# Optimization experiments

Measured on AMD Instinct MI355X. Metric: run time of the kernel, lower is better.

The kernel has to match this reference:

```python
import jax, jax.numpy as jnp
import numpy as np

V, H, L, NH, DH, FF, P, T = 21128, 768, 12, 12, 64, 3072, 512, 9
B, S = 16, 256
EPS = 1e-12

def _ln(x, g, b):
    m = x.mean(-1, keepdims=True)
    v = ((x - m) ** 2).mean(-1, keepdims=True)
    return (x - m) * jax.lax.rsqrt(v + EPS) * g + b

def setup_inputs() -> dict:
    key = jax.random.key(0)
    ks = iter(jax.random.split(key, 64))
    def nrm(shape, s=0.02):
        return (jax.random.normal(next(ks), shape, jnp.float32) * s)
    inp = {
        'input_ids': jax.random.randint(next(ks), (B, 1, S), 0, V, dtype=jnp.int32),
        'token_type_ids': jnp.zeros((B, 1, S), jnp.int32),
        'attention_mask': jnp.ones((B, 1, S), jnp.int32),
        'tags': jax.random.randint(next(ks), (B, S), 0, T, dtype=jnp.int32),
        'word_emb': nrm((V, H)), 'pos_emb': nrm((P, H)), 'type_emb': nrm((2, H)),
        'emb_ln_g': jnp.ones((H,), jnp.float32), 'emb_ln_b': jnp.zeros((H,), jnp.float32),
        'Wq': nrm((L, H, H)), 'bq': jnp.zeros((L, H), jnp.float32),
        'Wk': nrm((L, H, H)), 'bk': jnp.zeros((L, H), jnp.float32),
        'Wv': nrm((L, H, H)), 'bv': jnp.zeros((L, H), jnp.float32),
        'Wo': nrm((L, H, H)), 'bo': jnp.zeros((L, H), jnp.float32),
        'ln1_g': jnp.ones((L, H), jnp.float32), 'ln1_b': jnp.zeros((L, H), jnp.float32),
        'W1': nrm((L, H, FF)), 'b1': jnp.zeros((L, FF), jnp.float32),
        'W2': nrm((L, FF, H)), 'b2': jnp.zeros((L, H), jnp.float32),
        'ln2_g': jnp.ones((L, H), jnp.float32), 'ln2_b': jnp.zeros((L, H), jnp.float32),
        'dense_W': nrm((H, T)), 'dense_b': jnp.zeros((T,), jnp.float32),
        'crf_start': nrm((T,), 0.1), 'crf_end': nrm((T,), 0.1), 'crf_trans': nrm((T, T), 0.1),
    }
    return inp

def _model(input_ids, token_type_ids, attention_mask, tags,
           word_emb, pos_emb, type_emb, emb_ln_g, emb_ln_b,
           Wq, bq, Wk, bk, Wv, bv, Wo, bo, ln1_g, ln1_b,
           W1, b1, W2, b2, ln2_g, ln2_b, dense_W, dense_b,
           crf_start, crf_end, crf_trans):
    ids = input_ids[:, 0, :]            # [B,S]
    tt = token_type_ids[:, 0, :]
    amask = attention_mask[:, 0, :]     # [B,S] int
    Bn, Sn = ids.shape
    # --- BERT embeddings (post-LN BERT-base) ---
    x = word_emb[ids] + pos_emb[:Sn][None, :, :] + type_emb[tt]
    x = _ln(x, emb_ln_g, emb_ln_b)
    bias = jnp.where(amask[:, None, None, :] > 0, 0.0, -1e9).astype(x.dtype)  # [B,1,1,S]
    scale = 1.0 / np.sqrt(DH).astype(np.float32)
    def layer(h, p):
        wq, bq_, wk, bk_, wv, bv_, wo, bo_, g1, c1, w1, d1, w2, d2, g2, c2 = p
        q = (h @ wq + bq_).reshape(Bn, Sn, NH, DH).transpose(0, 2, 1, 3)
        k = (h @ wk + bk_).reshape(Bn, Sn, NH, DH).transpose(0, 2, 1, 3)
        v = (h @ wv + bv_).reshape(Bn, Sn, NH, DH).transpose(0, 2, 1, 3)
        att = jax.nn.softmax(jnp.einsum('bhqd,bhkd->bhqk', q, k) * scale + bias, axis=-1)
        ctx = jnp.einsum('bhqk,bhkd->bhqd', att, v).transpose(0, 2, 1, 3).reshape(Bn, Sn, H)
        h = _ln(h + ctx @ wo + bo_, g1, c1)
        ff = jax.nn.gelu(h @ w1 + d1, approximate=False)
        h = _ln(h + ff @ w2 + d2, g2, c2)
        return h, None
    x, _ = jax.lax.scan(layer, x, (Wq, bq, Wk, bk, Wv, bv, Wo, bo, ln1_g, ln1_b, W1, b1, W2, b2, ln2_g, ln2_b))
    # --- emission head, seq-first like the torch code ---
    emis = (x @ dense_W + dense_b).transpose(1, 0, 2)   # [S,B,T]
    m = (amask.T > 0)                                    # [S,B] bool
    tags_sb = tags.T                                     # [S,B]
    bidx = jnp.arange(Bn)
    # --- CRF numerator (gold path score) ---
    score0 = crf_start[tags_sb[0]] + emis[0, bidx, tags_sb[0]]
    def num_step(sc, inp):
        e, t, tp, mm = inp
        inc = crf_trans[tp, t] + e[bidx, t]
        return sc + jnp.where(mm, inc, 0.0), None
    score, _ = jax.lax.scan(num_step, score0, (emis[1:], tags_sb[1:], tags_sb[:-1], m[1:]))
    lengths = m.astype(jnp.int32).sum(0)                 # [B]
    last_tag = jnp.take_along_axis(tags_sb, (lengths - 1)[None, :], axis=0)[0]
    score = score + crf_end[last_tag]
    # --- CRF partition (forward algorithm) ---
    alpha0 = crf_start[None, :] + emis[0]                # [B,T]
    def fwd_step(a, inp):
        e, mm = inp
        nxt = jax.nn.logsumexp(a[:, :, None] + crf_trans[None, :, :] + e[:, None, :], axis=1)
        return jnp.where(mm[:, None], nxt, a), None
    alpha, _ = jax.lax.scan(fwd_step, alpha0, (emis[1:], m[1:]))
    logZ = jax.nn.logsumexp(alpha + crf_end[None, :], axis=-1)
    loss = -(score - logZ).mean()                        # reduction='mean'
    # --- Viterbi decode ---
    v0 = crf_start[None, :] + emis[0]
    tid = jnp.arange(T)
    def vit_step(vv, inp):
        e, mm = inp
        sc = vv[:, :, None] + crf_trans[None, :, :]       # [B,T,T]
        nv = sc.max(1) + e
        idx = sc.argmax(1).astype(jnp.int32)
        vv2 = jnp.where(mm[:, None], nv, vv)
        idx = jnp.where(mm[:, None], idx, tid[None, :].astype(jnp.int32))
        return vv2, idx
    vfin, hist = jax.lax.scan(vit_step, v0, (emis[1:], m[1:]))  # hist: [S-1,B,T]
    last = jnp.argmax(vfin + crf_end[None, :], axis=-1).astype(jnp.int32)  # [B]
    def back_step(t, h):
        prev = jnp.take_along_axis(h, t[:, None], axis=1)[:, 0]
        return prev, prev
    _, path = jax.lax.scan(back_step, last, hist, reverse=True)  # [S-1,B]
    preds = jnp.concatenate([path, last[None, :]], axis=0).T     # [B,S]
    return loss, preds

def reference(input_ids, token_type_ids, attention_mask, tags,
              word_emb, pos_emb, type_emb, emb_ln_g, emb_ln_b,
              Wq, bq, Wk, bk, Wv, bv, Wo, bo, ln1_g, ln1_b,
              W1, b1, W2, b2, ln2_g, ln2_b, dense_W, dense_b,
              crf_start, crf_end, crf_trans):
    return _model(input_ids, token_type_ids, attention_mask, tags,
                  word_emb, pos_emb, type_emb, emb_ln_g, emb_ln_b,
                  Wq, bq, Wk, bk, Wv, bv, Wo, bo, ln1_g, ln1_b,
                  W1, b1, W2, b2, ln2_g, ln2_b, dense_W, dense_b,
                  crf_start, crf_end, crf_trans)
```

## Files before the change

### kernel.cpp

```cpp
#include <hip/hip_runtime.h>
#include <math.h>

#define B_ 16
#define S_ 256
#define H_ 768
#define L_ 12
#define NH_ 12
#define DH_ 64
#define FF_ 3072
#define T_ 9

typedef unsigned short ushort_t;
typedef __attribute__((ext_vector_type(8))) __bf16 bf16x8;
typedef __attribute__((ext_vector_type(4))) float f32x4;
typedef __attribute__((ext_vector_type(4))) unsigned short us4;
typedef __attribute__((ext_vector_type(8))) unsigned short us8;
typedef __attribute__((ext_vector_type(4))) unsigned int u32x4;

__device__ __forceinline__ ushort_t f2bf(float f) {
  union { float f; unsigned u; } v; v.f = f;
  unsigned r = v.u + 0x7FFFu + ((v.u >> 16) & 1u);
  return (ushort_t)(r >> 16);
}
__device__ __forceinline__ float bf2f(ushort_t h) {
  union { unsigned u; float f; } v; v.u = ((unsigned)h) << 16;
  return v.f;
}
__device__ __forceinline__ float rdlane(float v, int l) {
  union { float f; int i; } u; u.f = v;
  union { int i; float f; } o; o.i = __builtin_amdgcn_readlane(u.i, l);
  return o.f;
}
__device__ __forceinline__ void gload16(const void* g, void* l) {
  __builtin_amdgcn_global_load_lds((const __attribute__((address_space(1))) void*)g,
                                   (__attribute__((address_space(3))) void*)l, 16, 0, 0);
}

__global__ __launch_bounds__(256) void emb_ln_kernel(const int* __restrict__ ids, const int* __restrict__ tt,
                              const float* __restrict__ we, const float* __restrict__ pe,
                              const float* __restrict__ te, const float* __restrict__ g,
                              const float* __restrict__ bb,
                              ushort_t* __restrict__ oh, ushort_t* __restrict__ ol) {
  const int token = blockIdx.x;
  const int tid = threadIdx.x;
  const int s = token & (S_ - 1);
  const int id = ids[token];
  const int t2 = tt[token];
  float x[3];
  float sum = 0.f;
#pragma unroll
  for (int i = 0; i < 3; ++i) {
    int d = tid + i * 256;
    x[i] = we[(size_t)id * H_ + d] + pe[(size_t)s * H_ + d] + te[(size_t)t2 * H_ + d];
    sum += x[i];
  }
  __shared__ float red[4];
#pragma unroll
  for (int o = 32; o > 0; o >>= 1) sum += __shfl_xor(sum, o, 64);
  const int wid = tid >> 6, lane = tid & 63;
  if (lane == 0) red[wid] = sum;
  __syncthreads();
  const float mean = (red[0] + red[1] + red[2] + red[3]) * (1.f / H_);
  float vs = 0.f;
#pragma unroll
  for (int i = 0; i < 3; ++i) { float dv = x[i] - mean; vs += dv * dv; }
#pragma unroll
  for (int o = 32; o > 0; o >>= 1) vs += __shfl_xor(vs, o, 64);
  __syncthreads();
  if (lane == 0) red[wid] = vs;
  __syncthreads();
  const float var = (red[0] + red[1] + red[2] + red[3]) * (1.f / H_);
  const float inv = rsqrtf(var + 1e-12f);
  ushort_t* hp = oh + (size_t)token * H_;
  ushort_t* lp = ol + (size_t)token * H_;
#pragma unroll
  for (int i = 0; i < 3; ++i) {
    int d = tid + i * 256;
    float y = (x[i] - mean) * inv * g[d] + bb[d];
    ushort_t h = f2bf(y);
    hp[d] = h;
    lp[d] = f2bf(y - bf2f(h));
  }
}

__global__ __launch_bounds__(256) void ln_kernel(const ushort_t* __restrict__ bh, const ushort_t* __restrict__ bl,
                          const float* __restrict__ delta,
                          const float* __restrict__ g, const float* __restrict__ bb,
                          ushort_t* __restrict__ oh, ushort_t* __restrict__ ol) {
  const int token = blockIdx.x;
  const int tid = threadIdx.x;
  const ushort_t* bhp = bh + (size_t)token * H_;
  const ushort_t* blp = bl + (size_t)token * H_;
  const float* dp = delta + (size_t)token * H_;
  float x[3];
  float s = 0.f;
#pragma unroll
  for (int i = 0; i < 3; ++i) {
    int d = tid + i * 256;
    x[i] = bf2f(bhp[d]) + bf2f(blp[d]) + dp[d];
    s += x[i];
  }
  __shared__ float red[4];
#pragma unroll
  for (int o = 32; o > 0; o >>= 1) s += __shfl_xor(s, o, 64);
  const int wid = tid >> 6, lane = tid & 63;
  if (lane == 0) red[wid] = s;
  __syncthreads();
  const float mean = (red[0] + red[1] + red[2] + red[3]) * (1.f / H_);
  float vs = 0.f;
#pragma unroll
  for (int i = 0; i < 3; ++i) { float dv = x[i] - mean; vs += dv * dv; }
#pragma unroll
  for (int o = 32; o > 0; o >>= 1) vs += __shfl_xor(vs, o, 64);
  __syncthreads();
  if (lane == 0) red[wid] = vs;
  __syncthreads();
  const float var = (red[0] + red[1] + red[2] + red[3]) * (1.f / H_);
  const float inv = rsqrtf(var + 1e-12f);
  ushort_t* hp = oh + (size_t)token * H_;
  ushort_t* lp = ol + (size_t)token * H_;
#pragma unroll
  for (int i = 0; i < 3; ++i) {
    int d = tid + i * 256;
    float y = (x[i] - mean) * inv * g[d] + bb[d];
    ushort_t h = f2bf(y);
    hp[d] = h;
    lp[d] = f2bf(y - bf2f(h));
  }
}

__global__ __launch_bounds__(256) void ln_emis_kernel(const ushort_t* __restrict__ bh, const ushort_t* __restrict__ bl,
                               const float* __restrict__ delta,
                               const float* __restrict__ g, const float* __restrict__ bb,
                               const float* __restrict__ W, const float* __restrict__ wbias,
                               float* __restrict__ E) {
  const int token = blockIdx.x;
  const int tid = threadIdx.x;
  __shared__ float sW[H_ * T_];
  __shared__ float red[4];
  __shared__ float wred[4][12];
  for (int i = tid; i < H_ * T_; i += 256) sW[i] = W[i];

  const ushort_t* bhp = bh + (size_t)token * H_;
  const ushort_t* blp = bl + (size_t)token * H_;
  const float* dp = delta + (size_t)token * H_;
  float x[3];
  float s = 0.f;
#pragma unroll
  for (int i = 0; i < 3; ++i) {
    int d = tid + i * 256;
    x[i] = bf2f(bhp[d]) + bf2f(blp[d]) + dp[d];
    s += x[i];
  }
#pragma unroll
  for (int o = 32; o > 0; o >>= 1) s += __shfl_xor(s, o, 64);
  const int wid = tid >> 6, lane = tid & 63;
  if (lane == 0) red[wid] = s;
  __syncthreads();
  const float mean = (red[0] + red[1] + red[2] + red[3]) * (1.f / H_);
  float vs = 0.f;
#pragma unroll
  for (int i = 0; i < 3; ++i) { float dv = x[i] - mean; vs += dv * dv; }
#pragma unroll
  for (int o = 32; o > 0; o >>= 1) vs += __shfl_xor(vs, o, 64);
  __syncthreads();
  if (lane == 0) red[wid] = vs;
  __syncthreads();
  const float var = (red[0] + red[1] + red[2] + red[3]) * (1.f / H_);
  const float inv = rsqrtf(var + 1e-12f);

  float acc9[T_];
#pragma unroll
  for (int t = 0; t < T_; ++t) acc9[t] = 0.f;
#pragma unroll
  for (int i = 0; i < 3; ++i) {
    int d = tid + i * 256;
    float y = (x[i] - mean) * inv * g[d] + bb[d];
    const float* wr = sW + d * T_;
#pragma unroll
    for (int t = 0; t < T_; ++t) acc9[t] = fmaf(y, wr[t], acc9[t]);
  }
#pragma unroll
  for (int o = 32; o > 0; o >>= 1)
#pragma unroll
    for (int t = 0; t < T_; ++t) acc9[t] += __shfl_xor(acc9[t], o, 64);
  if (lane == 0) {
#pragma unroll
    for (int t = 0; t < T_; ++t) wred[wid][t] = acc9[t];
  }
  __syncthreads();
  if (tid < T_) {
    const float v = wred[0][tid] + wred[1][tid] + wred[2][tid] + wred[3][tid] + wbias[tid];
    const int b2 = token >> 8, s2 = token & 255;
    E[((size_t)s2 * B_ + b2) * T_ + tid] = v;
  }
}

__device__ __forceinline__ void transpose_core(float (*t)[65], const float* __restrict__ src,
                                               ushort_t* __restrict__ dh,
                                               int K, int N, int n0, int k0) {
  const int tid = threadIdx.x;
#pragma unroll
  for (int i = 0; i < 16; ++i) {
    int lin = tid + i * 256;
    int kk = lin >> 6, nn = lin & 63;
    t[kk][nn] = src[(size_t)(k0 + kk) * N + n0 + nn];
  }
  __syncthreads();
#pragma unroll
  for (int i = 0; i < 16; ++i) {
    int lin = tid + i * 256;
    int nn = lin >> 6, kk = lin & 63;
    dh[(size_t)(n0 + nn) * K + k0 + kk] = f2bf(t[kk][nn]);
  }
}

__device__ __forceinline__ void wprep_dispatch(float (*t)[65], int wid,
                        const float* Wq, const float* Wk, const float* Wv, const float* Wo,
                        const float* W1, const float* W2,
                        ushort_t* WT4h, ushort_t* W1th, ushort_t* W2th) {
  if (wid < 576) {
    const int z = wid / 144, r = wid - z * 144;
    const int x = r % 12, y = r / 12;
    const float* src = z == 0 ? Wq : (z == 1 ? Wk : (z == 2 ? Wv : Wo));
    transpose_core(t, src, WT4h + (size_t)z * H_ * H_, H_, H_, x * 64, y * 64);
  } else if (wid < 1152) {
    const int i = wid - 576;
    const int x = i % 48, y = i / 48;
    transpose_core(t, W1, W1th, H_, FF_, x * 64, y * 64);
  } else {
    const int i = wid - 1152;
    const int x = i % 12, y = i / 12;
    transpose_core(t, W2, W2th, FF_, H_, x * 64, y * 64);
  }
}

__global__ __launch_bounds__(256) void wprep_k(const float* __restrict__ Wq, const float* __restrict__ Wk,
                        const float* __restrict__ Wv, const float* __restrict__ Wo,
                        const float* __restrict__ W1, const float* __restrict__ W2,
                        ushort_t* __restrict__ WT4h,
                        ushort_t* __restrict__ W1th, ushort_t* __restrict__ W2th) {
  __shared__ float t[64][65];
  wprep_dispatch(t, blockIdx.x, Wq, Wk, Wv, Wo, W1, W2, WT4h, W1th, W2th);
}

template <int R>
__device__ __forceinline__ void stage_slice(const ushort_t* __restrict__ gsrc, int K, char* lds) {
  const int tid = threadIdx.x;
  constexpr int NIT = (R * 4) / 256;
#pragma unroll
  for (int i = 0; i < NIT; ++i) {
    const int v = tid + i * 256;
    const int kh = v / (2 * R);
    const int r2 = v & (2 * R - 1);
    const int row = r2 >> 1;
    const int kg = (kh << 1) | ((r2 & 1) ^ ((row >> 2) & 1));
    gload16(gsrc + (size_t)row * K + kg * 8, lds + (i * 256 + (tid & 192)) * 16);
  }
}

template <int BM, int BN, int BK>
__device__ __forceinline__ void mgemm_acc(
    const ushort_t* __restrict__ Ah, const ushort_t* __restrict__ Al,
    const ushort_t* __restrict__ Bth,
    int K, f32x4 (&acc)[BM / 32][BN / 32], char* pool) {
  constexpr int FM = BM / 32;
  constexpr int FN = BN / 32;
  constexpr int ABYTES = BM * BK * 2;
  constexpr int BBYTES = BN * BK * 2;
  constexpr int BUF = 2 * ABYTES + BBYTES;
  constexpr int NL = (8 * BM + 4 * BN) / 256;
  const int tid = threadIdx.x;
  const int w = tid >> 6, lane = tid & 63;
  const int wm = w >> 1, wn = w & 1;
  const int kgL = lane >> 4, lr = lane & 15;
  const int row0 = blockIdx.y * BM, col0 = blockIdx.x * BN;

#pragma unroll
  for (int i = 0; i < FM; ++i)
#pragma unroll
    for (int j = 0; j < FN; ++j) acc[i][j] = (f32x4){0.f, 0.f, 0.f, 0.f};

  const int khL = kgL >> 1;
  const int swz = (((kgL & 1) ^ ((lr >> 2) & 1)) << 4);
  const int aB0 = khL * (BM * 32) + (wm * (BM / 2) + lr) * 32 + swz;
  const int bB0 = khL * (BN * 32) + (wn * (BN / 2) + lr) * 32 + swz;

  const ushort_t* gA_h = Ah + (size_t)row0 * K;
  const ushort_t* gA_l = Al + (size_t)row0 * K;
  const ushort_t* gB_h = Bth + (size_t)col0 * K;

  auto stageall = [&](int k0, char* buf) {
#pragma unroll
    for (int c = 0; c < BK / 32; ++c) {
      stage_slice<BM>(gA_h + k0 + c * 32, K, buf + c * BM * 64);
      stage_slice<BM>(gA_l + k0 + c * 32, K, buf + ABYTES + c * BM * 64);
      stage_slice<BN>(gB_h + k0 + c * 32, K, buf + 2 * ABYTES + c * BN * 64);
    }
  };

  const int nk = K / BK;
  stageall(0, pool);
  for (int k = 0; k < nk; ++k) {
    char* cur = pool + (k & 1) * BUF;
    if (k + 1 < nk) {
      stageall((k + 1) * BK, pool + ((k + 1) & 1) * BUF);
      if constexpr (NL == 6) {
        asm volatile("s_waitcnt vmcnt(6)" ::: "memory");
      } else if constexpr (NL == 8) {
        asm volatile("s_waitcnt vmcnt(8)" ::: "memory");
      } else {
        asm volatile("s_waitcnt vmcnt(0)" ::: "memory");
      }
    } else {
      asm volatile("s_waitcnt vmcnt(0)" ::: "memory");
    }
    __builtin_amdgcn_s_barrier();
    asm volatile("" ::: "memory");

#pragma unroll
    for (int ks = 0; ks < BK / 32; ++ks) {
      const char* aP = cur + ks * BM * 64;
      const char* bP = cur + 2 * ABYTES + ks * BN * 64;
      bf16x8 a_h[FM], a_l[FM], b_h[FN];
#pragma unroll
      for (int fm = 0; fm < FM; ++fm) {
        a_h[fm] = *(const bf16x8*)(aP + aB0 + fm * 512);
        a_l[fm] = *(const bf16x8*)(aP + ABYTES + aB0 + fm * 512);
      }
#pragma unroll
      for (int fn = 0; fn < FN; ++fn) {
        b_h[fn] = *(const bf16x8*)(bP + bB0 + fn * 512);
      }
#pragma unroll
      for (int fm = 0; fm < FM; ++fm)
#pragma unroll
        for (int fn = 0; fn < FN; ++fn) {
          f32x4 c = acc[fm][fn];
          c = __builtin_amdgcn_mfma_f32_16x16x32_bf16(a_h[fm], b_h[fn], c, 0, 0, 0);
          c = __builtin_amdgcn_mfma_f32_16x16x32_bf16(a_l[fm], b_h[fn], c, 0, 0, 0);
          acc[fm][fn] = c;
        }
    }
    asm volatile("" ::: "memory");
    __builtin_amdgcn_s_barrier();
  }
}

template <int BM, int BN, int BK, int EPI>
__global__ __launch_bounds__(256, 3) void mgemm(const ushort_t* __restrict__ Ah, const ushort_t* __restrict__ Al,
                      const ushort_t* __restrict__ Bth,
                      const float* __restrict__ bias, float* __restrict__ Cf,
                      ushort_t* __restrict__ Ch, ushort_t* __restrict__ Cl, int N, int K) {
  __shared__ __attribute__((aligned(16))) char pool[2 * (2 * BM * BK + BN * BK) * 2];
  f32x4 acc[BM / 32][BN / 32];
  mgemm_acc<BM, BN, BK>(Ah, Al, Bth, K, acc, pool);
  const int tid = threadIdx.x;
  const int w = tid >> 6, lane = tid & 63;
  const int wm = w >> 1, wn = w & 1;
  const int kg = lane >> 4, lr = lane & 15;
  const int row0 = blockIdx.y * BM, col0 = blockIdx.x * BN;
  float* tb = (float*)pool + w * (16 * 68);
  const int row0w = row0 + wm * (BM / 2);
  const int col0w = col0 + wn * (BN / 2);
#pragma unroll
  for (int fm = 0; fm < BM / 32; ++fm) {
#pragma unroll
    for (int fn = 0; fn < BN / 32; ++fn) {
      const int col = col0w + fn * 16 + lr;
      const float bv = bias[col];
#pragma unroll
      for (int r = 0; r < 4; ++r)
        tb[(kg * 4 + r) * 68 + fn * 16 + lr] = acc[fm][fn][r] + bv;
    }
#pragma unroll
    for (int it = 0; it < (BN / 16) / 8; ++it) {
      const int slot = it * 64 + lane;
      const int row16 = slot / (BN / 16);
      const int cg = slot % (BN / 16);
      const f32x4 a = *(const f32x4*)&tb[row16 * 68 + cg * 8];
      const f32x4 b2 = *(const f32x4*)&tb[row16 * 68 + cg * 8 + 4];
      const int grow = row0w + fm * 16 + row16;
      const size_t o = (size_t)grow * N + col0w + cg * 8;
      *(f32x4*)(Cf + o) = a;
      *(f32x4*)(Cf + o + 4) = b2;
    }
  }
}

__global__ __launch_bounds__(256, 2) void ff1_fused(
    const ushort_t* __restrict__ Xh, const ushort_t* __restrict__ Xl,
    const ushort_t* __restrict__ W1th, const float* __restrict__ bias,
    ushort_t* __restrict__ Ch, ushort_t* __restrict__ Cl,
    const float* __restrict__ WqN, const float* __restrict__ WkN,
    const float* __restrict__ WvN, const float* __restrict__ WoN,
    const float* __restrict__ W1N, const float* __restrict__ W2N,
    ushort_t* __restrict__ WT4hN, ushort_t* __restrict__ W1thN, ushort_t* __restrict__ W2thN) {
  __shared__ __attribute__((aligned(16))) char pool[2 * (2 * 128 * 32 + 256 * 32) * 2];
  if (blockIdx.y >= 32) {
    if (WqN == nullptr) return;
    const int wid = (blockIdx.y - 32) * 12 + blockIdx.x;
    wprep_dispatch((float(*)[65])pool, wid, WqN, WkN, WvN, WoN, W1N, W2N, WT4hN, W1thN, W2thN);
    return;
  }
  f32x4 acc[4][8];
  mgemm_acc<128, 256, 32>(Xh, Xl, W1th, H_, acc, pool);
  const int tid = threadIdx.x;
  const int w = tid >> 6, lane = tid & 63;
  const int wm = w >> 1, wn = w & 1;
  const int kg = lane >> 4, lr = lane & 15;
  const int row0 = blockIdx.y * 128, col0 = blockIdx.x * 256;
  unsigned* tb = (unsigned*)pool + w * (16 * 132);
  const int row0w = row0 + wm * 64;
  const int col0w = col0 + wn * 128;
#pragma unroll
  for (int fm = 0; fm < 4; ++fm) {
#pragma unroll
    for (int fn = 0; fn < 8; ++fn) {
      const int col = col0w + fn * 16 + lr;
      const float bv = bias[col];
#pragma unroll
      for (int r = 0; r < 4; ++r) {
        float v = acc[fm][fn][r] + bv;
        float gl = 0.5f * v * (1.f + erff(v * 0.70710678118654752f));
        ushort_t h = f2bf(gl);
        ushort_t lo = f2bf(gl - bf2f(h));
        tb[(kg * 4 + r) * 132 + fn * 16 + lr] = ((unsigned)h << 16) | lo;
      }
    }
#pragma unroll
    for (int it = 0; it < 4; ++it) {
      const int slot = it * 64 + lane;
      const int row16 = slot >> 4, cg = slot & 15;
      unsigned r8[8];
      *(u32x4*)&r8[0] = *(const u32x4*)&tb[row16 * 132 + cg * 8];
      *(u32x4*)&r8[4] = *(const u32x4*)&tb[row16 * 132 + cg * 8 + 4];
      us8 h8, l8;
#pragma unroll
      for (int j = 0; j < 8; ++j) {
        h8[j] = (ushort_t)(r8[j] >> 16);
        l8[j] = (ushort_t)(r8[j] & 0xffffu);
      }
      const int grow = row0w + fm * 16 + row16;
      const size_t o = (size_t)grow * FF_ + col0w + cg * 8;
      *(us8*)(Ch + o) = h8;
      *(us8*)(Cl + o) = l8;
    }
  }
}

__global__ __launch_bounds__(256) void qkv_m(const ushort_t* __restrict__ Xh, const ushort_t* __restrict__ Xl,
                      const ushort_t* __restrict__ WT4h,
                      const float* __restrict__ bq, const float* __restrict__ bk,
                      const float* __restrict__ bvv,
                      ushort_t* __restrict__ Qh, ushort_t* __restrict__ Ql,
                      ushort_t* __restrict__ Kh, ushort_t* __restrict__ Vth) {
  constexpr int ABYTES = 128 * 32 * 2;
  constexpr int BUF = 2 * ABYTES + 3 * ABYTES;
  __shared__ __attribute__((aligned(16))) char pool[2 * BUF];
  const int tid = threadIdx.x;
  const int w = tid >> 6, lane = tid & 63;
  const int wm = w >> 1, wn = w & 1;
  const int kgL = lane >> 4, lr = lane & 15;
  const int row0 = blockIdx.y * 128, col0 = blockIdx.x * 128;

  f32x4 acc[3][4][4];
#pragma unroll
  for (int z = 0; z < 3; ++z)
#pragma unroll
    for (int i = 0; i < 4; ++i)
#pragma unroll
      for (int j = 0; j < 4; ++j) acc[z][i][j] = (f32x4){0.f, 0.f, 0.f, 0.f};

  const int khL = kgL >> 1;
  const int swz = (((kgL & 1) ^ ((lr >> 2) & 1)) << 4);
  const int aB0 = khL * (128 * 32) + (wm * 64 + lr) * 32 + swz;
  const int bB0 = khL * (128 * 32) + (wn * 64 + lr) * 32 + swz;

  const ushort_t* gA_h = Xh + (size_t)row0 * H_;
  const ushort_t* gA_l = Xl + (size_t)row0 * H_;
  const ushort_t* gB0 = WT4h + (size_t)col0 * H_;
  const ushort_t* gB1 = WT4h + (size_t)H_ * H_ + (size_t)col0 * H_;
  const ushort_t* gB2 = WT4h + (size_t)2 * H_ * H_ + (size_t)col0 * H_;

  auto stageall = [&](int k0, char* buf) {
    stage_slice<128>(gA_h + k0, H_, buf);
    stage_slice<128>(gA_l + k0, H_, buf + ABYTES);
    stage_slice<128>(gB0 + k0, H_, buf + 2 * ABYTES);
    stage_slice<128>(gB1 + k0, H_, buf + 3 * ABYTES);
    stage_slice<128>(gB2 + k0, H_, buf + 4 * ABYTES);
  };

  const int nk = H_ / 32;
  stageall(0, pool);
  for (int k = 0; k < nk; ++k) {
    char* cur = pool + (k & 1) * BUF;
    if (k + 1 < nk) {
      stageall((k + 1) * 32, pool + ((k + 1) & 1) * BUF);
      asm volatile("s_waitcnt vmcnt(10)" ::: "memory");
    } else {
      asm volatile("s_waitcnt vmcnt(0)" ::: "memory");
    }
    __builtin_amdgcn_s_barrier();
    asm volatile("" ::: "memory");

    bf16x8 a_h[4], a_l[4];
#pragma unroll
    for (int fm = 0; fm < 4; ++fm) {
      a_h[fm] = *(const bf16x8*)(cur + aB0 + fm * 512);
      a_l[fm] = *(const bf16x8*)(cur + ABYTES + aB0 + fm * 512);
    }
#pragma unroll
    for (int z = 0; z < 3; ++z) {
      const char* bP = cur + (2 + z) * ABYTES;
      bf16x8 b_h[4];
#pragma unroll
      for (int fn = 0; fn < 4; ++fn) b_h[fn] = *(const bf16x8*)(bP + bB0 + fn * 512);
#pragma unroll
      for (int fm = 0; fm < 4; ++fm)
#pragma unroll
        for (int fn = 0; fn < 4; ++fn) {
          f32x4 c = acc[z][fm][fn];
          c = __builtin_amdgcn_mfma_f32_16x16x32_bf16(a_h[fm], b_h[fn], c, 0, 0, 0);
          c = __builtin_amdgcn_mfma_f32_16x16x32_bf16(a_l[fm], b_h[fn], c, 0, 0, 0);
          acc[z][fm][fn] = c;
        }
    }
    asm volatile("" ::: "memory");
    __builtin_amdgcn_s_barrier();
  }

  const int kg = kgL;
  unsigned* tb = (unsigned*)pool + w * (16 * 68);
  const int row0w = row0 + wm * 64;
  const int col0w = col0 + wn * 64;
#pragma unroll
  for (int z = 0; z < 2; ++z) {
    const float* bz = z == 0 ? bq : bk;
#pragma unroll
    for (int fm = 0; fm < 4; ++fm) {
#pragma unroll
      for (int fn = 0; fn < 4; ++fn) {
        const int col = col0w + fn * 16 + lr;
        const float bv = bz[col];
#pragma unroll
        for (int r = 0; r < 4; ++r) {
          float v = acc[z][fm][fn][r] + bv;
          ushort_t h = f2bf(v);
          ushort_t lo = f2bf(v - bf2f(h));
          tb[(kg * 4 + r) * 68 + fn * 16 + lr] = ((unsigned)h << 16) | lo;
        }
      }
#pragma unroll
      for (int it = 0; it < 2; ++it) {
        const int slot = it * 64 + lane;
        const int row16 = slot >> 3, cg = slot & 7;
        unsigned r8[8];
        *(u32x4*)&r8[0] = *(const u32x4*)&tb[row16 * 68 + cg * 8];
        *(u32x4*)&r8[4] = *(const u32x4*)&tb[row16 * 68 + cg * 8 + 4];
        us8 h8, l8;
#pragma unroll
        for (int j = 0; j < 8; ++j) {
          h8[j] = (ushort_t)(r8[j] >> 16);
          l8[j] = (ushort_t)(r8[j] & 0xffffu);
        }
        const int grow = row0w + fm * 16 + row16;
        const size_t o = (size_t)grow * H_ + col0w + cg * 8;
        if (z == 0) {
          *(us8*)(Qh + o) = h8;
          *(us8*)(Ql + o) = l8;
        } else {
          *(us8*)(Kh + o) = h8;
        }
      }
    }
  }
#pragma unroll
  for (int fn = 0; fn < 4; ++fn) {
    const int col = col0w + fn * 16 + lr;
    const float bv = bvv[col];
#pragma unroll
    for (int fm = 0; fm < 4; ++fm) {
      const int rowb = row0w + fm * 16 + kg * 4;
      us4 h4;
#pragma unroll
      for (int r = 0; r < 4; ++r) h4[r] = f2bf(acc[2][fm][fn][r] + bv);
      const int bb2 = rowb >> 8, s0 = rowb & 255;
      const int hh2 = col >> 6, d = col & 63;
      *(us4*)(Vth + ((size_t)(bb2 * NH_ + hh2) * DH_ + d) * S_ + s0) = h4;
    }
  }
}

__global__ __launch_bounds__(256, 3) void attn_mfma(
    const ushort_t* __restrict__ Qh, const ushort_t* __restrict__ Ql,
    const ushort_t* __restrict__ Kh, const ushort_t* __restrict__ Vth,
    const int* __restrict__ amask,
    ushort_t* __restrict__ Oh, ushort_t* __restrict__ Ol) {
  const int bid = blockIdx.x;
  const int qt = bid / 192;
  const int gh = bid - qt * 192;
  const int b = gh / NH_;
  const int h = gh - b * NH_;
  __shared__ __attribute__((aligned(16))) ushort_t sKh[2][64 * 64];
  __shared__ __attribute__((aligned(16))) ushort_t sVh[2][64 * 64];
  __shared__ __attribute__((aligned(16))) unsigned sP[4][16 * 68];
  __shared__ float sBias[2][64];
  const int tid = threadIdx.x;
  const int w = tid >> 6, lane = tid & 63;
  const int kg = lane >> 4, lr = lane & 15;

  const int qrow = b * S_ + qt * 64 + w * 16 + lr;
  bf16x8 qfh[2], qfl[2];
#pragma unroll
  for (int ds2 = 0; ds2 < 2; ++ds2) {
    const size_t off = (size_t)qrow * H_ + h * DH_ + ds2 * 32 + kg * 8;
    qfh[ds2] = *(const bf16x8*)(Qh + off);
    qfl[ds2] = *(const bf16x8*)(Ql + off);
  }

  f32x4 ctx[4];
#pragma unroll
  for (int i = 0; i < 4; ++i) ctx[i] = (f32x4){0.f, 0.f, 0.f, 0.f};
  float mrow[4], lrw[4];
#pragma unroll
  for (int r = 0; r < 4; ++r) { mrow[r] = -1e30f; lrw[r] = 0.f; }

  unsigned* sPw = &sP[w][0];

  auto stageKV = [&](int kt, int bufi) {
#pragma unroll
    for (int i = 0; i < 2; ++i) {
      const int v = tid + i * 256;
      const int row = v >> 3;
      const int c16 = (v & 7) ^ (row & 7);
      const size_t kgl = (size_t)(b * S_ + kt * 64 + row) * H_ + h * DH_ + c16 * 8;
      gload16(Kh + kgl, (char*)&sKh[bufi][0] + v * 16);
      const size_t vgl = (size_t)((b * NH_ + h) * DH_ + row) * S_ + kt * 64 + c16 * 8;
      gload16(Vth + vgl, (char*)&sVh[bufi][0] + v * 16);
    }
    if (tid < 64) sBias[bufi][tid] = (amask[b * S_ + kt * 64 + tid] > 0) ? 0.f : -1e9f;
  };

  stageKV(0, 0);
  for (int kt = 0; kt < 4; ++kt) {
    const int bi = kt & 1;
    if (kt < 3) {
      stageKV(kt + 1, bi ^ 1);
      asm volatile("s_waitcnt vmcnt(4) lgkmcnt(0)" ::: "memory");
    } else {
      asm volatile("s_waitcnt vmcnt(0) lgkmcnt(0)" ::: "memory");
    }
    __builtin_amdgcn_s_barrier();
    asm volatile("" ::: "memory");

    f32x4 sc[4];
#pragma unroll
    for (int kf = 0; kf < 4; ++kf) sc[kf] = (f32x4){0.f, 0.f, 0.f, 0.f};
#pragma unroll
    for (int kf = 0; kf < 4; ++kf) {
      const int krow = kf * 16 + lr;
#pragma unroll
      for (int ds2 = 0; ds2 < 2; ++ds2) {
        const int cb = (ds2 * 64 + kg * 16) ^ ((krow & 7) << 4);
        const bf16x8 kvh = *(const bf16x8*)((const char*)&sKh[bi][0] + krow * 128 + cb);
        sc[kf] = __builtin_amdgcn_mfma_f32_16x16x32_bf16(qfh[ds2], kvh, sc[kf], 0, 0, 0);
        sc[kf] = __builtin_amdgcn_mfma_f32_16x16x32_bf16(qfl[ds2], kvh, sc[kf], 0, 0, 0);
      }
    }
    float bsv[4];
#pragma unroll
    for (int kf = 0; kf < 4; ++kf) bsv[kf] = sBias[bi][kf * 16 + lr];

#pragma unroll
    for (int r = 0; r < 4; ++r) {
      float sv[4];
      float tmax = -1e30f;
#pragma unroll
      for (int kf = 0; kf < 4; ++kf) {
        sv[kf] = sc[kf][r] * 0.125f + bsv[kf];
        tmax = fmaxf(tmax, sv[kf]);
      }
#pragma unroll
      for (int o = 8; o > 0; o >>= 1) tmax = fmaxf(tmax, __shfl_xor(tmax, o, 64));
      const float mnew = fmaxf(mrow[r], tmax);
      const float corr = expf(mrow[r] - mnew);
      float ls = 0.f;
      const int qoff = (kg * 4 + r) * 68;
#pragma unroll
      for (int kf = 0; kf < 4; ++kf) {
        const float pe = expf(sv[kf] - mnew);
        ls += pe;
        const ushort_t hi = f2bf(pe);
        const ushort_t lo = f2bf(pe - bf2f(hi));
        sPw[qoff + kf * 16 + lr] = ((unsigned)hi << 16) | lo;
      }
#pragma unroll
      for (int o = 8; o > 0; o >>= 1) ls += __shfl_xor(ls, o, 64);
      lrw[r] = lrw[r] * corr + ls;
      mrow[r] = mnew;
#pragma unroll
      for (int df = 0; df < 4; ++df) ctx[df][r] *= corr;
    }

#pragma unroll
    for (int ks = 0; ks < 2; ++ks) {
      unsigned w8[8];
      *(u32x4*)&w8[0] = *(const u32x4*)(sPw + lr * 68 + ks * 32 + kg * 8);
      *(u32x4*)&w8[4] = *(const u32x4*)(sPw + lr * 68 + ks * 32 + kg * 8 + 4);
      union { bf16x8 v; ushort_t u[8]; } ph, pl;
#pragma unroll
      for (int j = 0; j < 8; ++j) { ph.u[j] = (ushort_t)(w8[j] >> 16); pl.u[j] = (ushort_t)(w8[j] & 0xffffu); }
#pragma unroll
      for (int df = 0; df < 4; ++df) {
        const int vrow = df * 16 + lr;
        const int cb = (ks * 64 + kg * 16) ^ ((vrow & 7) << 4);
        const bf16x8 vvh = *(const bf16x8*)((const char*)&sVh[bi][0] + vrow * 128 + cb);
        ctx[df] = __builtin_amdgcn_mfma_f32_16x16x32_bf16(ph.v, vvh, ctx[df], 0, 0, 0);
        ctx[df] = __builtin_amdgcn_mfma_f32_16x16x32_bf16(pl.v, vvh, ctx[df], 0, 0, 0);
      }
    }
    asm volatile("" ::: "memory");
    __builtin_amdgcn_s_barrier();
  }

#pragma unroll
  for (int r = 0; r < 4; ++r) {
    const float inv = 1.f / lrw[r];
    const int tok = b * S_ + qt * 64 + w * 16 + kg * 4 + r;
#pragma unroll
    for (int df = 0; df < 4; ++df) {
      const float v = ctx[df][r] * inv;
      const ushort_t hi = f2bf(v);
      const size_t o = (size_t)tok * H_ + h * DH_ + df * 16 + lr;
      Oh[o] = hi;
      Ol[o] = f2bf(v - bf2f(hi));
    }
  }
}

__global__ __launch_bounds__(128) void crf_kernel(const float* __restrict__ emis, const int* __restrict__ tags,
                          const int* __restrict__ amask,
                          const float* __restrict__ crf_start, const float* __restrict__ crf_end,
                          const float* __restrict__ trans,
                          float* __restrict__ partial, float* __restrict__ out) {
  const int b = blockIdx.x;
  const int tid = threadIdx.x;
  const int wv = tid >> 6;
  const int lane = tid & 63;
  __shared__ float sE[S_ * T_];
  __shared__ float sM[S_];
  __shared__ float trs[T_ * T_];
  __shared__ unsigned char hist[S_ - 1][16];
  __shared__ float pathf[S_];
  for (int i = tid; i < S_ * T_; i += 128) {
    const int s = i / T_, t = i - s * T_;
    sE[i] = emis[((size_t)s * B_ + b) * T_ + t];
  }
  for (int i = tid; i < S_; i += 128) sM[i] = (float)amask[b * S_ + i];
  for (int i = tid; i < T_ * T_; i += 128) trs[i] = trans[i];
  __syncthreads();

  const int t = lane;
  const bool act = t < T_;
  float trc[T_];
#pragma unroll
  for (int p = 0; p < T_; ++p) trc[p] = act ? trs[p * T_ + t] : 0.f;

  if (wv == 0) {
    float alpha = act ? crf_start[t] + sE[t] : 0.f;
    for (int s = 1; s < S_; ++s) {
      float ap[T_];
#pragma unroll
      for (int p = 0; p < T_; ++p) ap[p] = rdlane(alpha, p);
      if (act) {
        const float e = sE[s * T_ + t];
        float v[T_];
#pragma unroll
        for (int p = 0; p < T_; ++p) v[p] = ap[p] + trc[p];
        float m0 = fmaxf(fmaxf(v[0], v[1]), fmaxf(v[2], v[3]));
        float m1 = fmaxf(fmaxf(v[4], v[5]), fmaxf(v[6], v[7]));
        const float mx = fmaxf(fmaxf(m0, m1), v[8]);
        float sum = 0.f;
#pragma unroll
        for (int p = 0; p < T_; ++p) sum += __expf(v[p] - mx);
        const float na = mx + __logf(sum) + e;
        if (sM[s] > 0.f) alpha = na;
      }
    }
    float nsum = 0.f;
    int len = 0;
#pragma unroll
    for (int j = 0; j < 4; ++j) {
      const int s = lane + j * 64;
      const int mk = (sM[s] > 0.f) ? 1 : 0;
      len += mk;
      if (s >= 1 && mk) {
        const int tc = tags[b * S_ + s], tp = tags[b * S_ + s - 1];
        nsum += trs[tp * T_ + tc] + sE[s * T_ + tc];
      }
    }
#pragma unroll
    for (int o = 32; o > 0; o >>= 1) {
      nsum += __shfl_xor(nsum, o, 64);
      len += __shfl_xor(len, o, 64);
    }
    const float fz = act ? alpha + crf_end[t] : -1e30f;
    float zp[T_];
#pragma unroll
    for (int p = 0; p < T_; ++p) zp[p] = rdlane(fz, p);
    if (lane == 0) {
      float mx = -1e30f;
#pragma unroll
      for (int p = 0; p < T_; ++p) mx = fmaxf(mx, zp[p]);
      float sum = 0.f;
#pragma unroll
      for (int p = 0; p < T_; ++p) sum += __expf(zp[p] - mx);
      const float logZ = mx + __logf(sum);
      const int tg0 = tags[b * S_];
      const float score = nsum + crf_start[tg0] + sE[tg0] + crf_end[tags[b * S_ + len - 1]];
      partial[b] = score - logZ;
    }
  } else {
    float vit = act ? crf_start[t] + sE[t] : 0.f;
    for (int s = 1; s < S_; ++s) {
      float vp[T_];
#pragma unroll
      for (int p = 0; p < T_; ++p) vp[p] = rdlane(vit, p);
      if (act) {
        const float e = sE[s * T_ + t];
        float best = -1e30f; int bi = 0;
#pragma unroll
        for (int p = 0; p < T_; ++p) {
          const float scv = vp[p] + trc[p];
          if (scv > best) { best = scv; bi = p; }
        }
        if (sM[s] > 0.f) {
          vit = best + e;
          hist[s - 1][t] = (unsigned char)bi;
        } else {
          hist[s - 1][t] = (unsigned char)t;
        }
      }
    }
    const float fv = act ? vit + crf_end[t] : -1e30f;
    float wp[T_];
#pragma unroll
    for (int p = 0; p < T_; ++p) wp[p] = rdlane(fv, p);
    if (lane == 0) {
      float best = -1e30f; int lastTag = 0;
#pragma unroll
      for (int p = 0; p < T_; ++p) {
        if (wp[p] > best) { best = wp[p]; lastTag = p; }
      }
      int tc = lastTag;
      pathf[S_ - 1] = (float)tc;
      for (int i = S_ - 2; i >= 0; --i) {
        tc = hist[i][tc];
        pathf[i] = (float)tc;
      }
    }
  }
  __syncthreads();
#pragma unroll
  for (int j = 0; j < 2; ++j) {
    const int s = tid + j * 128;
    out[1 + b * S_ + s] = pathf[s];
  }
}

__global__ __launch_bounds__(64) void crf_final(const float* __restrict__ partial, float* __restrict__ out) {
  const int lane = threadIdx.x;
  float v = (lane < B_) ? partial[lane] : 0.f;
#pragma unroll
  for (int o = 32; o > 0; o >>= 1) v += __shfl_xor(v, o, 64);
  if (lane == 0) out[0] = -(v * (1.f / B_));
}

extern "C" void kernel_launch(void* const* d_in, const int* in_sizes, int n_in,
                              void* d_out, int out_size, void* d_ws, size_t ws_size,
                              hipStream_t stream) {
  const int* input_ids = (const int*)d_in[0];
  const int* token_type_ids = (const int*)d_in[1];
  const int* attention_mask = (const int*)d_in[2];
  const int* tags = (const int*)d_in[3];
  const float* word_emb = (const float*)d_in[4];
  const float* pos_emb = (const float*)d_in[5];
  const float* type_emb = (const float*)d_in[6];
  const float* emb_ln_g = (const float*)d_in[7];
  const float* emb_ln_b = (const float*)d_in[8];
  const float* Wq = (const float*)d_in[9];
  const float* bq = (const float*)d_in[10];
  const float* Wk = (const float*)d_in[11];
  const float* bk = (const float*)d_in[12];
  const float* Wv = (const float*)d_in[13];
  const float* bv = (const float*)d_in[14];
  const float* Wo = (const float*)d_in[15];
  const float* bo = (const float*)d_in[16];
  const float* ln1_g = (const float*)d_in[17];
  const float* ln1_b = (const float*)d_in[18];
  const float* W1 = (const float*)d_in[19];
  const float* b1 = (const float*)d_in[20];
  const float* W2 = (const float*)d_in[21];
  const float* b2 = (const float*)d_in[22];
  const float* ln2_g = (const float*)d_in[23];
  const float* ln2_b = (const float*)d_in[24];
  const float* dense_W = (const float*)d_in[25];
  const float* dense_b = (const float*)d_in[26];
  const float* crf_start = (const float*)d_in[27];
  const float* crf_end = (const float*)d_in[28];
  const float* crf_trans = (const float*)d_in[29];

  constexpr size_t NTOK = (size_t)B_ * S_;
  constexpr size_t XSZ = NTOK * H_;
  constexpr size_t WT4SZ = (size_t)4 * H_ * H_;
  constexpr size_t WFSZ = (size_t)H_ * FF_;

  char* p = (char*)d_ws;
  float* TMP = (float*)p;          p += XSZ * 4;
  char* UN = p;                    p += 8 * XSZ * 2;
  ushort_t* Qh = (ushort_t*)UN;
  ushort_t* Ql = Qh + XSZ;
  ushort_t* Kh = Ql + XSZ;
  ushort_t* Vth = Kh + XSZ;
  ushort_t* CTXh = Vth + XSZ;
  ushort_t* CTXl = CTXh + XSZ;
  ushort_t* FFh = (ushort_t*)UN;
  ushort_t* FFl = FFh + NTOK * FF_;
  ushort_t* Xh = (ushort_t*)p;     p += XSZ * 2;
  ushort_t* Xl = (ushort_t*)p;     p += XSZ * 2;
  ushort_t* WT4h2 = (ushort_t*)p;  p += WT4SZ * 2 * 2;
  ushort_t* W1th2 = (ushort_t*)p;  p += WFSZ * 2 * 2;
  ushort_t* W2th2 = (ushort_t*)p;  p += WFSZ * 2 * 2;
  float* EM = (float*)p;           p += (size_t)S_ * B_ * T_ * 4;
  float* PART = (float*)p;         p += B_ * 4;

  emb_ln_kernel<<<dim3(4096), dim3(256), 0, stream>>>(input_ids, token_type_ids, word_emb, pos_emb,
                                                      type_emb, emb_ln_g, emb_ln_b, Xh, Xl);
  wprep_k<<<dim3(1728), dim3(256), 0, stream>>>(Wq, Wk, Wv, Wo, W1, W2, WT4h2, W1th2, W2th2);

  for (int l = 0; l < L_; ++l) {
    const int pr = l & 1, pn = (l + 1) & 1;
    ushort_t* WT4h = WT4h2 + (size_t)pr * WT4SZ;
    ushort_t* W1th = W1th2 + (size_t)pr * WFSZ;
    ushort_t* W2th = W2th2 + (size_t)pr * WFSZ;
    const bool hasNext = (l + 1 < L_);
    const size_t wo_n = (size_t)(l + 1) * H_ * H_;

    qkv_m<<<dim3(6, 32), dim3(256), 0, stream>>>(Xh, Xl, WT4h, bq + (size_t)l * H_,
                                                 bk + (size_t)l * H_, bv + (size_t)l * H_,
                                                 Qh, Ql, Kh, Vth);
    attn_mfma<<<dim3(768), dim3(256), 0, stream>>>(Qh, Ql, Kh, Vth, attention_mask, CTXh, CTXl);
    mgemm<128, 128, 32, 0><<<dim3(6, 32), dim3(256), 0, stream>>>(
        CTXh, CTXl, WT4h + (size_t)3 * H_ * H_,
        bo + (size_t)l * H_, TMP, nullptr, nullptr, H_, H_);
    ln_kernel<<<dim3(4096), dim3(256), 0, stream>>>(Xh, Xl, TMP, ln1_g + (size_t)l * H_,
                                                    ln1_b + (size_t)l * H_, Xh, Xl);
    ff1_fused<<<dim3(12, 32 + 144), dim3(256), 0, stream>>>(
        Xh, Xl, W1th, b1 + (size_t)l * FF_, FFh, FFl,
        hasNext ? Wq + wo_n : nullptr, Wk + wo_n, Wv + wo_n, Wo + wo_n,
        W1 + (size_t)(l + 1) * WFSZ, W2 + (size_t)(l + 1) * WFSZ,
        WT4h2 + (size_t)pn * WT4SZ, W1th2 + (size_t)pn * WFSZ, W2th2 + (size_t)pn * WFSZ);
    mgemm<128, 128, 32, 0><<<dim3(6, 32), dim3(256), 0, stream>>>(
        FFh, FFl, W2th, b2 + (size_t)l * H_, TMP, nullptr, nullptr, H_, FF_);
    if (l + 1 < L_) {
      ln_kernel<<<dim3(4096), dim3(256), 0, stream>>>(Xh, Xl, TMP, ln2_g + (size_t)l * H_,
                                                      ln2_b + (size_t)l * H_, Xh, Xl);
    } else {
      ln_emis_kernel<<<dim3(4096), dim3(256), 0, stream>>>(Xh, Xl, TMP, ln2_g + (size_t)l * H_,
                                                           ln2_b + (size_t)l * H_, dense_W,
                                                           dense_b, EM);
    }
  }

  crf_kernel<<<dim3(B_), dim3(128), 0, stream>>>(EM, tags, attention_mask, crf_start, crf_end,
                                                 crf_trans, PART, (float*)d_out);
  crf_final<<<dim3(1), dim3(64), 0, stream>>>(PART, (float*)d_out);
}
```

Baseline: 3.064 ms.

## Remap GEMM block IDs across XCDs and prefetch CRF emissions

Remaps the linear block index in the generic GEMM, FF1 and QKV kernels so that consecutive tiles land on the same XCD (bid&7 chooses the chiplet group). The goal is better L2 reuse of shared A/B panels on the multi-die MI355X. Separately, the CRF forward and Viterbi loops prefetch the next step's emission and mask values from LDS to hide load latency on the serial recurrence. The remap assumes the grid size is divisible by 8, and tile order changes how work is balanced.

After: 2.795 ms. 1.1x faster.

```diff
diff --git a/kernel.cpp b/kernel.cpp
--- a/kernel.cpp
+++ b/kernel.cpp
@@ -263,7 +263,7 @@
 __device__ __forceinline__ void mgemm_acc(
     const ushort_t* __restrict__ Ah, const ushort_t* __restrict__ Al,
     const ushort_t* __restrict__ Bth,
-    int K, f32x4 (&acc)[BM / 32][BN / 32], char* pool) {
+    int K, f32x4 (&acc)[BM / 32][BN / 32], char* pool, int row0, int col0) {
   constexpr int FM = BM / 32;
   constexpr int FN = BN / 32;
   constexpr int ABYTES = BM * BK * 2;
@@ -274,7 +274,6 @@
   const int w = tid >> 6, lane = tid & 63;
   const int wm = w >> 1, wn = w & 1;
   const int kgL = lane >> 4, lr = lane & 15;
-  const int row0 = blockIdx.y * BM, col0 = blockIdx.x * BN;
 
 #pragma unroll
   for (int i = 0; i < FM; ++i)
@@ -353,13 +352,18 @@
                       const float* __restrict__ bias, float* __restrict__ Cf,
                       ushort_t* __restrict__ Ch, ushort_t* __restrict__ Cl, int N, int K) {
   __shared__ __attribute__((aligned(16))) char pool[2 * (2 * BM * BK + BN * BK) * 2];
+  const int ngem = gridDim.x * gridDim.y;
+  const int bid = blockIdx.x + blockIdx.y * gridDim.x;
+  const int cpx = ngem >> 3;
+  const int widb = (bid & 7) * cpx + (bid >> 3);
+  const int bx = widb % gridDim.x, by = widb / gridDim.x;
+  const int row0 = by * BM, col0 = bx * BN;
   f32x4 acc[BM / 32][BN / 32];
-  mgemm_acc<BM, BN, BK>(Ah, Al, Bth, K, acc, pool);
+  mgemm_acc<BM, BN, BK>(Ah, Al, Bth, K, acc, pool, row0, col0);
   const int tid = threadIdx.x;
   const int w = tid >> 6, lane = tid & 63;
   const int wm = w >> 1, wn = w & 1;
   const int kg = lane >> 4, lr = lane & 15;
-  const int row0 = blockIdx.y * BM, col0 = blockIdx.x * BN;
   float* tb = (float*)pool + w * (16 * 68);
   const int row0w = row0 + wm * (BM / 2);
   const int col0w = col0 + wn * (BN / 2);
@@ -403,13 +407,16 @@
     wprep_dispatch((float(*)[65])pool, wid, WqN, WkN, WvN, WoN, W1N, W2N, WT4hN, W1thN, W2thN);
     return;
   }
+  const int bid = blockIdx.x + blockIdx.y * 12;
+  const int widb = (bid & 7) * 48 + (bid >> 3);
+  const int bx = widb % 12, by = widb / 12;
+  const int row0 = by * 128, col0 = bx * 256;
   f32x4 acc[4][8];
-  mgemm_acc<128, 256, 32>(Xh, Xl, W1th, H_, acc, pool);
+  mgemm_acc<128, 256, 32>(Xh, Xl, W1th, H_, acc, pool, row0, col0);
   const int tid = threadIdx.x;
   const int w = tid >> 6, lane = tid & 63;
   const int wm = w >> 1, wn = w & 1;
   const int kg = lane >> 4, lr = lane & 15;
-  const int row0 = blockIdx.y * 128, col0 = blockIdx.x * 256;
   unsigned* tb = (unsigned*)pool + w * (16 * 132);
   const int row0w = row0 + wm * 64;
   const int col0w = col0 + wn * 128;
@@ -462,7 +469,10 @@
   const int w = tid >> 6, lane = tid & 63;
   const int wm = w >> 1, wn = w & 1;
   const int kgL = lane >> 4, lr = lane & 15;
-  const int row0 = blockIdx.y * 128, col0 = blockIdx.x * 128;
+  const int bid = blockIdx.x + blockIdx.y * 6;
+  const int widb = (bid & 7) * 24 + (bid >> 3);
+  const int bxs = widb % 6, bys = widb / 6;
+  const int row0 = bys * 128, col0 = bxs * 128;
 
   f32x4 acc[3][4][4];
 #pragma unroll
@@ -769,12 +779,18 @@
 
   if (wv == 0) {
     float alpha = act ? crf_start[t] + sE[t] : 0.f;
+    float eN = act ? sE[T_ + t] : 0.f;
+    float mN = sM[1];
     for (int s = 1; s < S_; ++s) {
+      const float e = eN, mm = mN;
+      if (s + 1 < S_) {
+        eN = act ? sE[(s + 1) * T_ + t] : 0.f;
+        mN = sM[s + 1];
+      }
       float ap[T_];
 #pragma unroll
       for (int p = 0; p < T_; ++p) ap[p] = rdlane(alpha, p);
       if (act) {
-        const float e = sE[s * T_ + t];
         float v[T_];
 #pragma unroll
         for (int p = 0; p < T_; ++p) v[p] = ap[p] + trc[p];
@@ -785,7 +801,7 @@
 #pragma unroll
         for (int p = 0; p < T_; ++p) sum += __expf(v[p] - mx);
         const float na = mx + __logf(sum) + e;
-        if (sM[s] > 0.f) alpha = na;
+        if (mm > 0.f) alpha = na;
       }
     }
     float nsum = 0.f;
@@ -823,19 +839,25 @@
     }
   } else {
     float vit = act ? crf_start[t] + sE[t] : 0.f;
+    float eN = act ? sE[T_ + t] : 0.f;
+    float mN = sM[1];
     for (int s = 1; s < S_; ++s) {
+      const float e = eN, mm = mN;
+      if (s + 1 < S_) {
+        eN = act ? sE[(s + 1) * T_ + t] : 0.f;
+        mN = sM[s + 1];
+      }
       float vp[T_];
 #pragma unroll
       for (int p = 0; p < T_; ++p) vp[p] = rdlane(vit, p);
       if (act) {
-        const float e = sE[s * T_ + t];
         float best = -1e30f; int bi = 0;
 #pragma unroll
         for (int p = 0; p < T_; ++p) {
           const float scv = vp[p] + trc[p];
           if (scv > best) { best = scv; bi = p; }
         }
-        if (sM[s] > 0.f) {
+        if (mm > 0.f) {
           vit = best + e;
           hist[s - 1][t] = (unsigned char)bi;
         } else {
```
